# Kernel optimization log

Measured on AMD Instinct MI355X. Metric: run time of the kernel, lower is better.

Reference implementation:

```python
import jax, jax.numpy as jnp
import numpy as np

S = 32   # parent grid side
G = 64   # child grid side (2*S)
C = 16   # channels
DN = ('NDHWC', 'DHWIO', 'NDHWC')


def conv3(t, w, b):
    # t: [D,H,W,Cin] dense grid; zero padding == nonexistent coords contribute 0 (ME semantics)
    return jax.lax.conv_general_dilated(t[None], w, (1, 1, 1), 'SAME', dimension_numbers=DN)[0] + b


def _grids():
    ix = jnp.arange(G)
    px = (ix % 2)[:, None, None]
    py = (ix % 2)[None, :, None]
    pz = (ix % 2)[None, None, :]
    oct_m = {(a, b, c): (px == a) & (py == b) & (pz == c)
             for a in (0, 1) for b in (0, 1) for c in (0, 1)}
    groups6 = [[(0, 0, 0)], [(1, 1, 0)], [(1, 0, 1)], [(0, 1, 1)],
               [(1, 0, 0), (0, 1, 0)], [(0, 0, 1), (1, 1, 1)]]
    g6 = [jnp.any(jnp.stack([oct_m[o] for o in g]), 0) for g in groups6]
    s3 = (ix // 2)[:, None, None] + (ix // 2)[None, :, None] + (ix // 2)[None, None, :]
    m3 = [(s3 % 3) == j for j in range(3)]  # 3-way repartition (group_mask_gen_par)
    return g6, m3


def coder(feat, occ, w1, b1, w2, b2):
    # ProbCoder: conv -> ReLU -> conv -> sigmoid; outputs exist only at input coords
    of = occ[..., None].astype(feat.dtype)
    h = jax.nn.relu(conv3(feat, w1, b1)) * of
    return jax.nn.sigmoid(conv3(h, w2, b2)) * of


def union(a, b):
    (fa, oa), (fb, ob) = a, b
    return (jnp.where(oa[..., None], fa, fb), oa | ob)


def _forward(x, w_down, b_down, w_fel1, b_fel1, w_fel2, b_fel2, w_up, b_up,
             wc1, bc1, wc2, bc2, wl1, bl1, wl2, bl2):
    g6, m3 = _grids()
    occ_x = x[..., 0] > 0                                    # GT occupied child voxels
    # down (stride-2 conv): coordinate effect only -- last_POV uses ones_like features
    p_occ = jnp.any(occ_x.reshape(S, 2, S, 2, S, 2), axis=(1, 3, 5))  # parent coords
    pf = p_occ[..., None].astype(x.dtype)                    # last_POV features (ones)
    # FEL (dfa): conv(1->C,k3)+ReLU+conv(C->C,k3), outputs only at existing parents
    h = jax.nn.relu(conv3(pf, w_fel1, b_fel1)) * pf
    h = conv3(h, w_fel2, b_fel2) * pf                        # [S,S,S,C]
    # generative transposed conv k2 s2: each parent emits 8 children (octant-specific weight)
    up = jnp.einsum('xyzc,ocd->xyzod', h, w_up) + b_up       # [S,S,S,8,C]
    up = up.reshape(S, S, S, 2, 2, 2, C).transpose(0, 3, 1, 4, 2, 5, 6).reshape(G, G, G, C)
    occ = jnp.repeat(jnp.repeat(jnp.repeat(p_occ, 2, 0), 2, 1), 2, 2)  # child coords of prob
    prob_f = up * occ[..., None]
    lab = [occ_x & g for g in g6]                            # generate_label: GT per group
    # ---------- anchor1 compression (3 sub-stages inside octant group 1) ----------
    a1_o = occ & g6[0]
    a1_f = prob_f * a1_o[..., None]
    r = [(a1_f * m[..., None], a1_o & m) for m in m3]
    lab1 = [lab[0] & m for m in m3]
    p11 = coder(r[0][0], r[0][1], wc1[0], bc1[0], wc2[0], bc2[0])
    d1s = (prob_f * lab1[0][..., None], lab1[0])             # decoded GT of sub-stage 1
    in2 = union(r[1], d1s)
    p12 = coder(in2[0], in2[1], wl1[0], bl1[0], wl2[0], bl2[0]) * (in2[1] & m3[1])[..., None]
    d2s = (prob_f * lab1[1][..., None], lab1[1])
    in3 = union(union(d1s, d2s), r[2])
    p13 = coder(in3[0], in3[1], wl1[1], bl1[1], wl2[1], bl2[1]) * (in3[1] & m3[2])[..., None]
    # ---------- anchors 2..6 ----------
    dec = (prob_f * lab[0][..., None], lab[0])               # prob_anchor1_dec
    probs = [p11, p12, p13]
    for k in range(1, 6):
        ak_o = occ & g6[k]
        ak = (prob_f * ak_o[..., None], ak_o)
        inp = union(dec, ak)
        pk = coder(inp[0], inp[1], wc1[k], bc1[k], wc2[k], bc2[k]) * (inp[1] & g6[k])[..., None]
        probs.append(pk)
        if k < 5:
            dk = (prob_f * lab[k][..., None], lab[k])
            dec = union(dec, dk)
    probs = jnp.stack([p[..., 0] for p in probs], 0)          # [8,G,G,G]
    labels = jnp.stack([lab1[0], lab1[1], lab1[2], lab[1], lab[2], lab[3], lab[4], lab[5]], 0).astype(x.dtype)
    return probs, labels


def setup_inputs() -> dict:
    key = jax.random.key(0)
    ks = jax.random.split(key, 20)
    f = lambda k, s: jax.random.normal(k, s, jnp.float32) * 0.1
    x = (jax.random.uniform(ks[0], (G, G, G, 1)) < 0.5).astype(jnp.float32)
    return {
        'x': x,
        'w_down': f(ks[1], (2, 2, 2, 1, 1)), 'b_down': f(ks[2], (1,)),
        'w_fel1': f(ks[3], (3, 3, 3, 1, C)), 'b_fel1': f(ks[4], (C,)),
        'w_fel2': f(ks[5], (3, 3, 3, C, C)), 'b_fel2': f(ks[6], (C,)),
        'w_up': f(ks[7], (8, C, C)), 'b_up': f(ks[8], (C,)),
        'wc1': f(ks[9], (6, 3, 3, 3, C, C)), 'bc1': f(ks[10], (6, C)),
        'wc2': f(ks[11], (6, 3, 3, 3, C, 1)), 'bc2': f(ks[12], (6, 1)),
        'wl1': f(ks[13], (2, 5, 5, 5, C, C)), 'bl1': f(ks[14], (2, C)),
        'wl2': f(ks[15], (2, 5, 5, 5, C, 1)), 'bl2': f(ks[16], (2, 1)),
    }


def reference(x, w_down, b_down, w_fel1, b_fel1, w_fel2, b_fel2, w_up, b_up,
              wc1, bc1, wc2, bc2, wl1, bl1, wl2, bl2):
    return _forward(x, w_down, b_down, w_fel1, b_fel1, w_fel2, b_fel2, w_up, b_up,
                    wc1, bc1, wc2, bc2, wl1, bl1, wl2, bl2)
```

## Files before the change

### kernel.cpp

```cpp
#include <hip/hip_runtime.h>
#include <cstdint>
#include <math.h>

#define G 64
#define S 32
#define G3 (G*G*G)
#define S3 (S*S*S)

typedef unsigned long long u64;
typedef unsigned int u32;

__device__ __forceinline__ float sigmoidf_(float v) {
    return 1.0f / (1.0f + expf(-v));
}
__device__ __forceinline__ u32 f2bf_rne(float f) {
    u32 u = __float_as_uint(f);
    u += 0x7fff + ((u >> 16) & 1);
    return u >> 16;
}

__global__ __launch_bounds__(256) void k_pocc(const float* __restrict__ x,
                                              unsigned char* __restrict__ pocc) {
    int p = blockIdx.x * 256 + threadIdx.x;
    if (p >= S3) return;
    int pz = p & 31, py = (p >> 5) & 31, px = p >> 10;
    const float* b = x + (((size_t)(px * 2) * G + py * 2) * G + pz * 2);
    bool occ = false;
    #pragma unroll
    for (int a = 0; a < 2; a++)
        #pragma unroll
        for (int bb = 0; bb < 2; bb++)
            #pragma unroll
            for (int c = 0; c < 2; c++)
                occ = occ || (b[((size_t)a * G + bb) * G + c] > 0.0f);
    pocc[p] = occ ? 1 : 0;
}

__global__ __launch_bounds__(256) void k_fel1(const unsigned char* __restrict__ pocc,
                                              const float* __restrict__ w1,
                                              const float* __restrict__ b1,
                                              float* __restrict__ h1) {
    int p = blockIdx.x * 256 + threadIdx.x;
    if (p >= S3) return;
    int pz = p & 31, py = (p >> 5) & 31, px = p >> 10;
    float* o = h1 + (size_t)p * 16;
    if (!pocc[p]) {
        #pragma unroll
        for (int i = 0; i < 16; i++) o[i] = 0.0f;
        return;
    }
    float acc[16];
    #pragma unroll
    for (int i = 0; i < 16; i++) acc[i] = b1[i];
    for (int dx = -1; dx <= 1; ++dx) {
        int nx = px + dx; if ((unsigned)nx >= S) continue;
        for (int dy = -1; dy <= 1; ++dy) {
            int ny = py + dy; if ((unsigned)ny >= S) continue;
            for (int dz = -1; dz <= 1; ++dz) {
                int nz = pz + dz; if ((unsigned)nz >= S) continue;
                if (pocc[(nx * S + ny) * S + nz]) {
                    const float* w = w1 + (((dx + 1) * 3 + (dy + 1)) * 3 + (dz + 1)) * 16;
                    #pragma unroll
                    for (int i = 0; i < 16; i++) acc[i] += w[i];
                }
            }
        }
    }
    #pragma unroll
    for (int i = 0; i < 16; i++) o[i] = fmaxf(acc[i], 0.0f);
}

__global__ __launch_bounds__(256) void k_fel2(const unsigned char* __restrict__ pocc,
                                              const float* __restrict__ h1,
                                              const float* __restrict__ w2,
                                              const float* __restrict__ b2,
                                              float* __restrict__ h2) {
    int p = blockIdx.x * 256 + threadIdx.x;
    if (p >= S3) return;
    int pz = p & 31, py = (p >> 5) & 31, px = p >> 10;
    float* o = h2 + (size_t)p * 16;
    if (!pocc[p]) {
        #pragma unroll
        for (int i = 0; i < 16; i++) o[i] = 0.0f;
        return;
    }
    float acc[16];
    #pragma unroll
    for (int i = 0; i < 16; i++) acc[i] = b2[i];
    for (int dx = -1; dx <= 1; ++dx) {
        int nx = px + dx; if ((unsigned)nx >= S) continue;
        for (int dy = -1; dy <= 1; ++dy) {
            int ny = py + dy; if ((unsigned)ny >= S) continue;
            for (int dz = -1; dz <= 1; ++dz) {
                int nz = pz + dz; if ((unsigned)nz >= S) continue;
                const float* f = h1 + (size_t)((nx * S + ny) * S + nz) * 16;
                const float* w = w2 + (((dx + 1) * 3 + (dy + 1)) * 3 + (dz + 1)) * 256;
                #pragma unroll
                for (int ci = 0; ci < 16; ++ci) {
                    float fv = f[ci];
                    #pragma unroll
                    for (int co = 0; co < 16; ++co)
                        acc[co] = fmaf(fv, w[ci * 16 + co], acc[co]);
                }
            }
        }
    }
    #pragma unroll
    for (int i = 0; i < 16; i++) o[i] = acc[i];
}

__global__ __launch_bounds__(256) void k_up(const unsigned char* __restrict__ pocc,
                                            const float* __restrict__ h2,
                                            const float* __restrict__ wup,
                                            const float* __restrict__ bup,
                                            float* __restrict__ prob_f) {
    int p = blockIdx.x * 256 + threadIdx.x;
    if (p >= S3) return;
    int pz = p & 31, py = (p >> 5) & 31, px = p >> 10;
    bool occ = pocc[p] != 0;
    float h[16];
    const float* hp = h2 + (size_t)p * 16;
    #pragma unroll
    for (int i = 0; i < 16; i++) h[i] = hp[i];
    #pragma unroll
    for (int o = 0; o < 8; o++) {
        int a = o >> 2, b = (o >> 1) & 1, c = o & 1;
        float* op = prob_f + (((size_t)(2 * px + a) * G + (2 * py + b)) * G + (2 * pz + c)) * 16;
        if (!occ) {
            #pragma unroll
            for (int d = 0; d < 16; d++) op[d] = 0.0f;
        } else {
            #pragma unroll
            for (int d = 0; d < 16; d++) {
                float acc = bup[d];
                #pragma unroll
                for (int cc = 0; cc < 16; cc++)
                    acc = fmaf(h[cc], wup[(o * 16 + cc) * 16 + d], acc);
                op[d] = acc;
            }
        }
    }
}

__global__ __launch_bounds__(256) void k_masks(const float* __restrict__ x,
                                               const unsigned char* __restrict__ pocc,
                                               u64* __restrict__ lw_in,
                                               u64* __restrict__ lw_fin,
                                               float* __restrict__ labels) {
    int z = threadIdx.x;
    int y = blockIdx.x * 4 + threadIdx.y;
    int xx = blockIdx.y;
    int v = (xx * G + y) * G + z;
    int par = ((xx & 1) << 2) | ((y & 1) << 1) | (z & 1);
    const int gmap[8] = {0, 5, 4, 3, 4, 2, 1, 5};
    int g = gmap[par];
    int t = ((xx >> 1) + (y >> 1) + (z >> 1)) % 3;
    bool occ = pocc[(((xx >> 1) * S) + (y >> 1)) * S + (z >> 1)] != 0;
    bool ox = x[v] > 0.0f;
    bool g0 = (g == 0);

    bool mi[8], mf[8], lb[8];
    mi[0] = occ && g0 && (t == 0);
    mi[1] = (occ && g0 && (t == 1)) || (ox && g0 && (t == 0));
    mi[2] = (ox && g0 && (t < 2)) || (occ && g0 && (t == 2));
    mi[3] = (ox && g0)       || (occ && (g == 1));
    mi[4] = (ox && (g <= 1)) || (occ && (g == 2));
    mi[5] = (ox && (g <= 2)) || (occ && (g == 3));
    mi[6] = (ox && (g <= 3)) || (occ && (g == 4));
    mi[7] = (ox && (g <= 4)) || (occ && (g == 5));

    mf[0] = occ && g0 && (t == 0);
    mf[1] = occ && g0 && (t == 1);
    mf[2] = occ && g0 && (t == 2);
    mf[3] = occ && (g == 1);
    mf[4] = occ && (g == 2);
    mf[5] = occ && (g == 3);
    mf[6] = occ && (g == 4);
    mf[7] = occ && (g == 5);

    lb[0] = ox && g0 && (t == 0);
    lb[1] = ox && g0 && (t == 1);
    lb[2] = ox && g0 && (t == 2);
    lb[3] = ox && (g == 1);
    lb[4] = ox && (g == 2);
    lb[5] = ox && (g == 3);
    lb[6] = ox && (g == 4);
    lb[7] = ox && (g == 5);

    int line = xx * G + y;
    #pragma unroll
    for (int c = 0; c < 8; ++c) {
        u64 wi = __ballot((int)mi[c]);
        u64 wf = __ballot((int)mf[c]);
        if (z == 0) {
            lw_in[c * 4096 + line] = wi;
            lw_fin[c * 4096 + line] = wf;
        }
        labels[(size_t)c * G3 + v] = lb[c] ? 1.0f : 0.0f;
    }
}

__device__ __forceinline__ u64 tap_hit(u64 wout, u64 wn, int dz) {
    return (dz >= 0) ? (wout & (wn >> dz)) : (wout & (wn << (-dz)));
}

template <int KS>
__device__ __forceinline__ void conv1_body(const float* __restrict__ prob_f,
                                           const u64* __restrict__ lw,
                                           const float* __restrict__ w1,
                                           const float* __restrict__ b1,
                                           u32* __restrict__ h_c) {
    const int R = KS / 2;
    int z = threadIdx.x;
    int line = blockIdx.x * 4 + threadIdx.y;
    int xx = line >> 6, y = line & 63;
    u64 w0 = lw[line];
    if (w0 == 0ULL) return;
    bool m = (w0 >> z) & 1;

    float acc[16];
    #pragma unroll
    for (int i = 0; i < 16; i++) acc[i] = b1[i];

    for (int dx = -R; dx <= R; ++dx) {
        int nx = xx + dx; if ((unsigned)nx >= G) continue;
        for (int dy = -R; dy <= R; ++dy) {
            int ny = y + dy; if ((unsigned)ny >= G) continue;
            u64 wn = lw[nx * G + ny];
            if (wn == 0ULL) continue;
            const float* wbase = w1 + (size_t)(((dx + R) * KS + (dy + R)) * KS) * 256;
            #pragma unroll
            for (int dz = -R; dz <= R; ++dz) {
                if (tap_hit(w0, wn, dz) == 0ULL) continue;
                int nz = z + dz;
                bool ok = (unsigned)nz < G;
                int nzc = ok ? nz : 0;
                bool mn = ok && ((wn >> nzc) & 1);
                const float4* f4 = reinterpret_cast<const float4*>(
                    prob_f + ((size_t)((nx * G + ny) * G + nzc)) * 16);
                float4 A = f4[0], B4 = f4[1], C4 = f4[2], D4 = f4[3];
                if (!mn) { A = make_float4(0, 0, 0, 0); B4 = A; C4 = A; D4 = A; }
                float fr[16] = {A.x, A.y, A.z, A.w, B4.x, B4.y, B4.z, B4.w,
                                C4.x, C4.y, C4.z, C4.w, D4.x, D4.y, D4.z, D4.w};
                const float* w = wbase + (dz + R) * 256;
                #pragma unroll
                for (int ci = 0; ci < 16; ++ci) {
                    float fv = fr[ci];
                    #pragma unroll
                    for (int co = 0; co < 16; ++co)
                        acc[co] = fmaf(fv, w[ci * 16 + co], acc[co]);
                }
            }
        }
    }
    if (m) {
        u32 pk[8];
        #pragma unroll
        for (int i = 0; i < 8; ++i) {
            u32 lo = f2bf_rne(fmaxf(acc[2 * i], 0.0f));
            u32 hi = f2bf_rne(fmaxf(acc[2 * i + 1], 0.0f));
            pk[i] = lo | (hi << 16);
        }
        uint4* o4 = reinterpret_cast<uint4*>(h_c + ((size_t)((xx * G + y) * G + z)) * 8);
        o4[0] = make_uint4(pk[0], pk[1], pk[2], pk[3]);
        o4[1] = make_uint4(pk[4], pk[5], pk[6], pk[7]);
    }
}

template <int KS>
__device__ __forceinline__ void conv2_body(const u32* __restrict__ h_c,
                                           const u64* __restrict__ lwi,
                                           const u64* __restrict__ lwf,
                                           const float* __restrict__ w2,
                                           const float* __restrict__ b2,
                                           float* __restrict__ outp) {
    const int R = KS / 2;
    int z = threadIdx.x;
    int line = blockIdx.x * 4 + threadIdx.y;
    int xx = line >> 6, y = line & 63;
    int v = (xx * G + y) * G + z;
    u64 wf = lwf[line];
    if (wf == 0ULL) { outp[v] = 0.0f; return; }
    bool m = (wf >> z) & 1;

    float acc = b2[0];
    for (int dx = -R; dx <= R; ++dx) {
        int nx = xx + dx; if ((unsigned)nx >= G) continue;
        for (int dy = -R; dy <= R; ++dy) {
            int ny = y + dy; if ((unsigned)ny >= G) continue;
            u64 wn = lwi[nx * G + ny];
            if (wn == 0ULL) continue;
            const float* wbase = w2 + (size_t)(((dx + R) * KS + (dy + R)) * KS) * 16;
            #pragma unroll
            for (int dz = -R; dz <= R; ++dz) {
                if (tap_hit(wf, wn, dz) == 0ULL) continue;
                int nz = z + dz;
                bool ok = (unsigned)nz < G;
                int nzc = ok ? nz : 0;
                bool mn = ok && ((wn >> nzc) & 1);
                const uint4* h4 = reinterpret_cast<const uint4*>(
                    h_c + ((size_t)((nx * G + ny) * G + nzc)) * 8);
                uint4 Ua = h4[0], Ub = h4[1];
                u32 uu[8] = {Ua.x, Ua.y, Ua.z, Ua.w, Ub.x, Ub.y, Ub.z, Ub.w};
                const float* w = wbase + (dz + R) * 16;
                if (mn) {
                    #pragma unroll
                    for (int i = 0; i < 8; ++i) {
                        float lo = __uint_as_float(uu[i] << 16);
                        float hi = __uint_as_float(uu[i] & 0xffff0000u);
                        acc = fmaf(lo, w[2 * i], acc);
                        acc = fmaf(hi, w[2 * i + 1], acc);
                    }
                }
            }
        }
    }
    outp[v] = m ? sigmoidf_(acc) : 0.0f;
}

__global__ __launch_bounds__(256) void k_conv1_all(const float* __restrict__ prob_f,
                                                   const u64* __restrict__ lw_in,
                                                   const float* __restrict__ wc1,
                                                   const float* __restrict__ bc1,
                                                   const float* __restrict__ wl1,
                                                   const float* __restrict__ bl1,
                                                   u32* __restrict__ hbase,
                                                   int coderBase) {
    int c = coderBase + blockIdx.y;
    const u64* lw = lw_in + (size_t)c * 4096;
    u32* h_c = hbase + (size_t)blockIdx.y * G3 * 8;
    if (c == 1 || c == 2) {
        conv1_body<5>(prob_f, lw, wl1 + (size_t)(c - 1) * 32000, bl1 + (c - 1) * 16, h_c);
    } else {
        int j = (c == 0) ? 0 : (c - 2);
        conv1_body<3>(prob_f, lw, wc1 + (size_t)j * 6912, bc1 + j * 16, h_c);
    }
}

__global__ __launch_bounds__(256) void k_conv2_all(const u32* __restrict__ hbase,
                                                   const u64* __restrict__ lw_in,
                                                   const u64* __restrict__ lw_fin,
                                                   const float* __restrict__ wc2,
                                                   const float* __restrict__ bc2,
                                                   const float* __restrict__ wl2,
                                                   const float* __restrict__ bl2,
                                                   float* __restrict__ out,
                                                   int coderBase) {
    int c = coderBase + blockIdx.y;
    const u64* lwi = lw_in + (size_t)c * 4096;
    const u64* lwf = lw_fin + (size_t)c * 4096;
    const u32* h_c = hbase + (size_t)blockIdx.y * G3 * 8;
    float* outp = out + (size_t)c * G3;
    if (c == 1 || c == 2) {
        conv2_body<5>(h_c, lwi, lwf, wl2 + (size_t)(c - 1) * 2000, bl2 + (c - 1), outp);
    } else {
        int j = (c == 0) ? 0 : (c - 2);
        conv2_body<3>(h_c, lwi, lwf, wc2 + (size_t)j * 432, bc2 + j, outp);
    }
}

extern "C" void kernel_launch(void* const* d_in, const int* in_sizes, int n_in,
                              void* d_out, int out_size, void* d_ws, size_t ws_size,
                              hipStream_t stream) {
    const float* x      = (const float*)d_in[0];
    const float* w_fel1 = (const float*)d_in[3];
    const float* b_fel1 = (const float*)d_in[4];
    const float* w_fel2 = (const float*)d_in[5];
    const float* b_fel2 = (const float*)d_in[6];
    const float* w_up   = (const float*)d_in[7];
    const float* b_up   = (const float*)d_in[8];
    const float* wc1    = (const float*)d_in[9];
    const float* bc1    = (const float*)d_in[10];
    const float* wc2    = (const float*)d_in[11];
    const float* bc2    = (const float*)d_in[12];
    const float* wl1    = (const float*)d_in[13];
    const float* bl1    = (const float*)d_in[14];
    const float* wl2    = (const float*)d_in[15];
    const float* bl2    = (const float*)d_in[16];
    float* out = (float*)d_out;

    char* ws = (char*)d_ws;
    float* prob_f = (float*)(ws);
    float* h1     = (float*)(ws + 16777216);
    float* h2     = (float*)(ws + 18874368);
    unsigned char* pocc = (unsigned char*)(ws + 20971520);
    u64* lw_in  = (u64*)(ws + 21004288);
    u64* lw_fin = (u64*)(ws + 21266432);
    u32* hbase  = (u32*)(ws + 21528576);

    const size_t fixed_end = 21528576;
    const size_t hsz = (size_t)G3 * 16 * 2;
    int B = 2;
    if (fixed_end + 8 * hsz <= ws_size) B = 8;
    else if (fixed_end + 4 * hsz <= ws_size) B = 4;

    k_pocc <<<dim3(S3 / 256), dim3(256), 0, stream>>>(x, pocc);
    k_fel1 <<<dim3(S3 / 256), dim3(256), 0, stream>>>(pocc, w_fel1, b_fel1, h1);
    k_fel2 <<<dim3(S3 / 256), dim3(256), 0, stream>>>(pocc, h1, w_fel2, b_fel2, h2);
    k_up   <<<dim3(S3 / 256), dim3(256), 0, stream>>>(pocc, h2, w_up, b_up, prob_f);
    k_masks<<<dim3(16, 64), dim3(64, 4), 0, stream>>>(x, pocc, lw_in, lw_fin, out + (size_t)8 * G3);

    for (int b0 = 0; b0 < 8; b0 += B) {
        int nb = (8 - b0 < B) ? (8 - b0) : B;
        k_conv1_all<<<dim3(1024, nb), dim3(64, 4), 0, stream>>>(
            prob_f, lw_in, wc1, bc1, wl1, bl1, hbase, b0);
        k_conv2_all<<<dim3(1024, nb), dim3(64, 4), 0, stream>>>(
            hbase, lw_in, lw_fin, wc2, bc2, wl2, bl2, out, b0);
    }
}
```

Baseline: 258.8 us.

## Run coder conv1 on bf16 MFMA with LDS-staged z-lines and prepacked weights

Replaces the scalar FMA first coder convolution with a matrix-core version. Each wave computes a 64-voxel z-line as four 16x16 tiles using bf16 MFMA, with two z-taps packed into the K=32 dimension. The neighbour feature lines are staged in LDS per dx, and the weight fragments are prepacked by a new kernel. The upsampled features are now stored as bf16, which halves their footprint and bandwidth, and conv2 now skips loads for empty neighbours. The cost is lower precision in prob features, extra barriers, and scalar per-element stores of the output.

```diff
diff --git a/kernel.cpp b/kernel.cpp
--- a/kernel.cpp
+++ b/kernel.cpp
@@ -9,6 +9,10 @@
 
 typedef unsigned long long u64;
 typedef unsigned int u32;
+typedef unsigned short u16;
+
+typedef __attribute__((ext_vector_type(8))) short s16x8;
+typedef __attribute__((ext_vector_type(4))) float f32x4;
 
 __device__ __forceinline__ float sigmoidf_(float v) {
     return 1.0f / (1.0f + expf(-v));
@@ -17,6 +21,14 @@
     u32 u = __float_as_uint(f);
     u += 0x7fff + ((u >> 16) & 1);
     return u >> 16;
+}
+__device__ __forceinline__ u64 rfl64(u64 v) {
+    u32 lo = __builtin_amdgcn_readfirstlane((u32)v);
+    u32 hi = __builtin_amdgcn_readfirstlane((u32)(v >> 32));
+    return ((u64)hi << 32) | lo;
+}
+__device__ __forceinline__ u64 tap_hit(u64 wout, u64 wn, int dz) {
+    return (dz >= 0) ? (wout & (wn >> dz)) : (wout & (wn << (-dz)));
 }
 
 __global__ __launch_bounds__(256) void k_pocc(const float* __restrict__ x,
@@ -113,7 +125,7 @@
                                             const float* __restrict__ h2,
                                             const float* __restrict__ wup,
                                             const float* __restrict__ bup,
-                                            float* __restrict__ prob_f) {
+                                            u16* __restrict__ probf16) {
     int p = blockIdx.x * 256 + threadIdx.x;
     if (p >= S3) return;
     int pz = p & 31, py = (p >> 5) & 31, px = p >> 10;
@@ -125,19 +137,25 @@
     #pragma unroll
     for (int o = 0; o < 8; o++) {
         int a = o >> 2, b = (o >> 1) & 1, c = o & 1;
-        float* op = prob_f + (((size_t)(2 * px + a) * G + (2 * py + b)) * G + (2 * pz + c)) * 16;
+        u16* op = probf16 + (((size_t)(2 * px + a) * G + (2 * py + b)) * G + (2 * pz + c)) * 16;
+        uint4* o4 = reinterpret_cast<uint4*>(op);
         if (!occ) {
+            o4[0] = make_uint4(0, 0, 0, 0);
+            o4[1] = make_uint4(0, 0, 0, 0);
+        } else {
+            u32 pk[8];
             #pragma unroll
-            for (int d = 0; d < 16; d++) op[d] = 0.0f;
-        } else {
-            #pragma unroll
-            for (int d = 0; d < 16; d++) {
-                float acc = bup[d];
+            for (int i = 0; i < 8; ++i) {
+                float a0 = bup[2 * i], a1 = bup[2 * i + 1];
                 #pragma unroll
-                for (int cc = 0; cc < 16; cc++)
-                    acc = fmaf(h[cc], wup[(o * 16 + cc) * 16 + d], acc);
-                op[d] = acc;
-            }
+                for (int cc = 0; cc < 16; cc++) {
+                    a0 = fmaf(h[cc], wup[(o * 16 + cc) * 16 + 2 * i], a0);
+                    a1 = fmaf(h[cc], wup[(o * 16 + cc) * 16 + 2 * i + 1], a1);
+                }
+                pk[i] = f2bf_rne(a0) | (f2bf_rne(a1) << 16);
+            }
+            o4[0] = make_uint4(pk[0], pk[1], pk[2], pk[3]);
+            o4[1] = make_uint4(pk[4], pk[5], pk[6], pk[7]);
         }
     }
 }
@@ -200,70 +218,148 @@
     }
 }
 
-__device__ __forceinline__ u64 tap_hit(u64 wout, u64 wn, int dz) {
-    return (dz >= 0) ? (wout & (wn >> dz)) : (wout & (wn << (-dz)));
-}
-
-template <int KS>
-__device__ __forceinline__ void conv1_body(const float* __restrict__ prob_f,
-                                           const u64* __restrict__ lw,
-                                           const float* __restrict__ w1,
-                                           const float* __restrict__ b1,
-                                           u32* __restrict__ h_c) {
-    const int R = KS / 2;
-    int z = threadIdx.x;
-    int line = blockIdx.x * 4 + threadIdx.y;
-    int xx = line >> 6, y = line & 63;
-    u64 w0 = lw[line];
+#define FRAGSTRIDE 38400
+__global__ __launch_bounds__(64) void k_prep_bfrag(const float* __restrict__ wc1,
+                                                   const float* __restrict__ wl1,
+                                                   u16* __restrict__ bfrag) {
+    int c = blockIdx.x;
+    int frag = blockIdx.y;
+    int lane = threadIdx.x;
+    bool is5 = (c == 1 || c == 2);
+    int R = is5 ? 2 : 1;
+    int KS = 2 * R + 1;
+    int npair = R + 1;
+    int nfrag = KS * KS * npair;
+    if (frag >= nfrag) return;
+    const float* W = is5 ? (wl1 + (size_t)(c - 1) * 32000)
+                         : (wc1 + (size_t)((c == 0) ? 0 : (c - 2)) * 6912);
+    int dxdy = frag / npair, p = frag - dxdy * npair;
+    int dxi = dxdy / KS, dyi = dxdy - dxi * KS;
+    int dziA = 2 * p, dziB = 2 * p + 1;
+    int co = lane & 15, kg = lane >> 4;
+    u16 outv[8];
+    #pragma unroll
+    for (int j = 0; j < 8; ++j) {
+        int k = kg * 8 + j;
+        int ci = k & 15;
+        int dzi = (k < 16) ? dziA : dziB;
+        float v = 0.0f;
+        if (dzi < KS)
+            v = W[(size_t)((dxi * KS + dyi) * KS + dzi) * 256 + ci * 16 + co];
+        outv[j] = (u16)f2bf_rne(v);
+    }
+    u16* o = bfrag + (size_t)c * FRAGSTRIDE + ((size_t)frag * 64 + lane) * 8;
+    uint4 pk;
+    pk.x = outv[0] | ((u32)outv[1] << 16);
+    pk.y = outv[2] | ((u32)outv[3] << 16);
+    pk.z = outv[4] | ((u32)outv[5] << 16);
+    pk.w = outv[6] | ((u32)outv[7] << 16);
+    *reinterpret_cast<uint4*>(o) = pk;
+}
+
+__global__ __launch_bounds__(256) void k_conv1_mfma(const u16* __restrict__ probf16,
+                                                    const u64* __restrict__ lw_in,
+                                                    const u16* __restrict__ bfrag,
+                                                    const float* __restrict__ bc1,
+                                                    const float* __restrict__ bl1,
+                                                    u16* __restrict__ hbase,
+                                                    int coderBase) {
+    int c = coderBase + blockIdx.y;
+    bool is5 = (c == 1 || c == 2);
+    int R = is5 ? 2 : 1;
+    int KS = 2 * R + 1, npair = R + 1;
+    const u64* lw = lw_in + (size_t)c * 4096;
+    u16* h_c = hbase + (size_t)blockIdx.y * G3 * 16;
+    const u16* bf = bfrag + (size_t)c * FRAGSTRIDE;
+    const float* bptr = is5 ? (bl1 + (c - 1) * 16)
+                            : (bc1 + ((c == 0) ? 0 : (c - 2)) * 16);
+
+    int x = blockIdx.x >> 4;
+    int y0 = (blockIdx.x & 15) << 2;
+    int w = threadIdx.y;
+    int lane = threadIdx.x;
+    int yw = y0 + w;
+
+    u64 w0 = rfl64(lw[x * G + yw]);
+    u64 anyw = lw[x * G + y0] | lw[x * G + y0 + 1] | lw[x * G + y0 + 2] | lw[x * G + y0 + 3];
+    if (anyw == 0ULL) return;
+
+    __shared__ u32 lds[8 * 2304 / 4];
+
+    int col = lane & 15, kg = lane >> 4;
+    float bv = bptr[col];
+    f32x4 acc[4];
+    #pragma unroll
+    for (int s = 0; s < 4; ++s) acc[s] = (f32x4){bv, bv, bv, bv};
+
+    int nlines = 4 + 2 * R;
+    int nunits = nlines * 144;
+    int t = w * 64 + lane;
+
+    for (int dx = -R; dx <= R; ++dx) {
+        int nx = x + dx;
+        __syncthreads();
+        if ((unsigned)nx < G) {
+            for (int u = t; u < nunits; u += 256) {
+                int s = u / 144; int q = u - s * 144;
+                int lz = q >> 1, half = q & 1;
+                int gz = lz - 4;
+                int ny = y0 - R + s;
+                uint4 val = make_uint4(0, 0, 0, 0);
+                if ((unsigned)ny < G && (unsigned)gz < G) {
+                    u64 wn = lw[nx * G + ny];
+                    if ((wn >> gz) & 1)
+                        val = *reinterpret_cast<const uint4*>(
+                            probf16 + ((size_t)((nx * G + ny) * G + gz) * 16 + half * 8));
+                }
+                *reinterpret_cast<uint4*>(
+                    reinterpret_cast<char*>(lds) + s * 2304 + half * 1152 + lz * 16) = val;
+            }
+        }
+        __syncthreads();
+        if (w0 == 0ULL || (unsigned)nx >= G) continue;
+
+        for (int dy = -R; dy <= R; ++dy) {
+            int ny = yw + dy;
+            if ((unsigned)ny >= G) continue;
+            u64 wn = rfl64(lw[nx * G + ny]);
+            if (wn == 0ULL) continue;
+            int slot = w + dy + R;
+            for (int p = 0; p < npair; ++p) {
+                int dzA = -R + 2 * p;
+                int dzB = dzA + 1;
+                bool hasB = (dzB <= R);
+                u64 hit = tap_hit(w0, wn, dzA);
+                if (hasB) hit |= tap_hit(w0, wn, dzB);
+                if (hit == 0ULL) continue;
+                int frag = ((dx + R) * KS + (dy + R)) * npair + p;
+                s16x8 bf8 = *reinterpret_cast<const s16x8*>(bf + ((size_t)frag * 64 + lane) * 8);
+                int dz = (kg < 2) ? dzA : (hasB ? dzB : dzA);
+                int lzb = (lane & 15) + dz + 4;
+                const char* abase = reinterpret_cast<const char*>(lds)
+                                    + slot * 2304 + (kg & 1) * 1152;
+                #pragma unroll
+                for (int s = 0; s < 4; ++s) {
+                    if (((hit >> (s * 16)) & 0xFFFFULL) == 0ULL) continue;
+                    s16x8 a = *reinterpret_cast<const s16x8*>(abase + (s * 16 + lzb) * 16);
+                    acc[s] = __builtin_amdgcn_mfma_f32_16x16x32_bf16(a, bf8, acc[s], 0, 0, 0);
+                }
+            }
+        }
+    }
+
     if (w0 == 0ULL) return;
-    bool m = (w0 >> z) & 1;
-
-    float acc[16];
-    #pragma unroll
-    for (int i = 0; i < 16; i++) acc[i] = b1[i];
-
-    for (int dx = -R; dx <= R; ++dx) {
-        int nx = xx + dx; if ((unsigned)nx >= G) continue;
-        for (int dy = -R; dy <= R; ++dy) {
-            int ny = y + dy; if ((unsigned)ny >= G) continue;
-            u64 wn = lw[nx * G + ny];
-            if (wn == 0ULL) continue;
-            const float* wbase = w1 + (size_t)(((dx + R) * KS + (dy + R)) * KS) * 256;
-            #pragma unroll
-            for (int dz = -R; dz <= R; ++dz) {
-                if (tap_hit(w0, wn, dz) == 0ULL) continue;
-                int nz = z + dz;
-                bool ok = (unsigned)nz < G;
-                int nzc = ok ? nz : 0;
-                bool mn = ok && ((wn >> nzc) & 1);
-                const float4* f4 = reinterpret_cast<const float4*>(
-                    prob_f + ((size_t)((nx * G + ny) * G + nzc)) * 16);
-                float4 A = f4[0], B4 = f4[1], C4 = f4[2], D4 = f4[3];
-                if (!mn) { A = make_float4(0, 0, 0, 0); B4 = A; C4 = A; D4 = A; }
-                float fr[16] = {A.x, A.y, A.z, A.w, B4.x, B4.y, B4.z, B4.w,
-                                C4.x, C4.y, C4.z, C4.w, D4.x, D4.y, D4.z, D4.w};
-                const float* w = wbase + (dz + R) * 256;
-                #pragma unroll
-                for (int ci = 0; ci < 16; ++ci) {
-                    float fv = fr[ci];
-                    #pragma unroll
-                    for (int co = 0; co < 16; ++co)
-                        acc[co] = fmaf(fv, w[ci * 16 + co], acc[co]);
-                }
-            }
-        }
-    }
-    if (m) {
-        u32 pk[8];
+    u16* hline = h_c + (size_t)(x * G + yw) * G * 16;
+    #pragma unroll
+    for (int s = 0; s < 4; ++s) {
         #pragma unroll
-        for (int i = 0; i < 8; ++i) {
-            u32 lo = f2bf_rne(fmaxf(acc[2 * i], 0.0f));
-            u32 hi = f2bf_rne(fmaxf(acc[2 * i + 1], 0.0f));
-            pk[i] = lo | (hi << 16);
-        }
-        uint4* o4 = reinterpret_cast<uint4*>(h_c + ((size_t)((xx * G + y) * G + z)) * 8);
-        o4[0] = make_uint4(pk[0], pk[1], pk[2], pk[3]);
-        o4[1] = make_uint4(pk[4], pk[5], pk[6], pk[7]);
+        for (int r = 0; r < 4; ++r) {
+            int z = s * 16 + kg * 4 + r;
+            if ((w0 >> z) & 1) {
+                float v = fmaxf(acc[s][r], 0.0f);
+                hline[z * 16 + col] = (u16)f2bf_rne(v);
+            }
+        }
     }
 }
 
@@ -279,7 +375,7 @@
     int line = blockIdx.x * 4 + threadIdx.y;
     int xx = line >> 6, y = line & 63;
     int v = (xx * G + y) * G + z;
-    u64 wf = lwf[line];
+    u64 wf = rfl64(lwf[line]);
     if (wf == 0ULL) { outp[v] = 0.0f; return; }
     bool m = (wf >> z) & 1;
 
@@ -288,7 +384,7 @@
         int nx = xx + dx; if ((unsigned)nx >= G) continue;
         for (int dy = -R; dy <= R; ++dy) {
             int ny = y + dy; if ((unsigned)ny >= G) continue;
-            u64 wn = lwi[nx * G + ny];
+            u64 wn = rfl64(lwi[nx * G + ny]);
             if (wn == 0ULL) continue;
             const float* wbase = w2 + (size_t)(((dx + R) * KS + (dy + R)) * KS) * 16;
             #pragma unroll
@@ -298,12 +394,12 @@
                 bool ok = (unsigned)nz < G;
                 int nzc = ok ? nz : 0;
                 bool mn = ok && ((wn >> nzc) & 1);
-                const uint4* h4 = reinterpret_cast<const uint4*>(
-                    h_c + ((size_t)((nx * G + ny) * G + nzc)) * 8);
-                uint4 Ua = h4[0], Ub = h4[1];
-                u32 uu[8] = {Ua.x, Ua.y, Ua.z, Ua.w, Ub.x, Ub.y, Ub.z, Ub.w};
                 const float* w = wbase + (dz + R) * 16;
                 if (mn) {
+                    const uint4* h4 = reinterpret_cast<const uint4*>(
+                        h_c + ((size_t)((nx * G + ny) * G + nzc)) * 8);
+                    uint4 Ua = h4[0], Ub = h4[1];
+                    u32 uu[8] = {Ua.x, Ua.y, Ua.z, Ua.w, Ub.x, Ub.y, Ub.z, Ub.w};
                     #pragma unroll
                     for (int i = 0; i < 8; ++i) {
                         float lo = __uint_as_float(uu[i] << 16);
@@ -316,25 +412,6 @@
         }
     }
     outp[v] = m ? sigmoidf_(acc) : 0.0f;
-}
-
-__global__ __launch_bounds__(256) void k_conv1_all(const float* __restrict__ prob_f,
-                                                   const u64* __restrict__ lw_in,
-                                                   const float* __restrict__ wc1,
-                                                   const float* __restrict__ bc1,
-                                                   const float* __restrict__ wl1,
-                                                   const float* __restrict__ bl1,
-                                                   u32* __restrict__ hbase,
-                                                   int coderBase) {
-    int c = coderBase + blockIdx.y;
-    const u64* lw = lw_in + (size_t)c * 4096;
-    u32* h_c = hbase + (size_t)blockIdx.y * G3 * 8;
-    if (c == 1 || c == 2) {
-        conv1_body<5>(prob_f, lw, wl1 + (size_t)(c - 1) * 32000, bl1 + (c - 1) * 16, h_c);
-    } else {
-        int j = (c == 0) ? 0 : (c - 2);
-        conv1_body<3>(prob_f, lw, wc1 + (size_t)j * 6912, bc1 + j * 16, h_c);
-    }
 }
 
 __global__ __launch_bounds__(256) void k_conv2_all(const u32* __restrict__ hbase,
@@ -380,15 +457,16 @@
     float* out = (float*)d_out;
 
     char* ws = (char*)d_ws;
-    float* prob_f = (float*)(ws);
-    float* h1     = (float*)(ws + 16777216);
-    float* h2     = (float*)(ws + 18874368);
-    unsigned char* pocc = (unsigned char*)(ws + 20971520);
-    u64* lw_in  = (u64*)(ws + 21004288);
-    u64* lw_fin = (u64*)(ws + 21266432);
-    u32* hbase  = (u32*)(ws + 21528576);
-
-    const size_t fixed_end = 21528576;
+    u16*  probf16 = (u16*)(ws);
+    float* h1     = (float*)(ws + 8388608);
+    float* h2     = (float*)(ws + 10485760);
+    unsigned char* pocc = (unsigned char*)(ws + 12582912);
+    u64* lw_in  = (u64*)(ws + 12615680);
+    u64* lw_fin = (u64*)(ws + 12877824);
+    u16* bfrag  = (u16*)(ws + 13139968);
+    u16* hbase  = (u16*)(ws + 13754368);
+
+    const size_t fixed_end = 13754368;
     const size_t hsz = (size_t)G3 * 16 * 2;
     int B = 2;
     if (fixed_end + 8 * hsz <= ws_size) B = 8;
@@ -397,14 +475,15 @@
     k_pocc <<<dim3(S3 / 256), dim3(256), 0, stream>>>(x, pocc);
     k_fel1 <<<dim3(S3 / 256), dim3(256), 0, stream>>>(pocc, w_fel1, b_fel1, h1);
     k_fel2 <<<dim3(S3 / 256), dim3(256), 0, stream>>>(pocc, h1, w_fel2, b_fel2, h2);
-    k_up   <<<dim3(S3 / 256), dim3(256), 0, stream>>>(pocc, h2, w_up, b_up, prob_f);
+    k_up   <<<dim3(S3 / 256), dim3(256), 0, stream>>>(pocc, h2, w_up, b_up, probf16);
     k_masks<<<dim3(16, 64), dim3(64, 4), 0, stream>>>(x, pocc, lw_in, lw_fin, out + (size_t)8 * G3);
+    k_prep_bfrag<<<dim3(8, 75), dim3(64), 0, stream>>>(wc1, wl1, bfrag);
 
     for (int b0 = 0; b0 < 8; b0 += B) {
         int nb = (8 - b0 < B) ? (8 - b0) : B;
-        k_conv1_all<<<dim3(1024, nb), dim3(64, 4), 0, stream>>>(
-            prob_f, lw_in, wc1, bc1, wl1, bl1, hbase, b0);
+        k_conv1_mfma<<<dim3(1024, nb), dim3(64, 4), 0, stream>>>(
+            probf16, lw_in, bfrag, bc1, bl1, hbase, b0);
         k_conv2_all<<<dim3(1024, nb), dim3(64, 4), 0, stream>>>(
-            hbase, lw_in, lw_fin, wc2, bc2, wl2, bl2, out, b0);
-    }
-}
+            (const u32*)hbase, lw_in, lw_fin, wc2, bc2, wl2, bl2, out, b0);
+    }
+}
```

Result: faster. 212.1 us (-18.0%).
